# Performance work log

Hardware: AMD Instinct MI355X
Metric: run time of the kernel (lower is better)

Reference implementation:

```python
import jax, jax.numpy as jnp
import numpy as np

B, N, E, H = 32, 1024, 1024, 8
D = E // H      # head_dim = 128, att_mid_dim = [128, 64, 128]
MID = 64


def setup_inputs() -> dict:
    key = jax.random.key(0)
    ks = jax.random.split(key, 12)

    def lin(k, out_d, in_d):
        return (jax.random.normal(k, (out_d, in_d), jnp.float32) * 0.02,
                jnp.zeros((out_d,), jnp.float32))

    Wq, bq = lin(ks[0], E, E)
    Wk, bk = lin(ks[1], E, E)
    Wv, bv = lin(ks[2], E, E)
    Wb, bb = lin(ks[3], MID, D)    # attention_basic: Linear(mid[0]=D -> mid[1]=64) + ReLU
    Wl, bl = lin(ks[4], 1, MID)    # attention_last: Linear(64 -> 1)
    Wl2, bl2 = lin(ks[5], D, MID)  # attention_last2: Linear(64 -> D)
    query = jax.random.normal(ks[6], (B, E), jnp.float32)
    k_in = jax.random.normal(ks[7], (B, N, E), jnp.float32)
    value1 = jax.random.normal(ks[8], (B, E), jnp.float32)
    value2 = jax.random.normal(ks[9], (B, N, E), jnp.float32)
    mask = jax.random.randint(ks[10], (B, N), 0, 2, jnp.int32)
    mask = mask.at[:, 0].set(1)  # guarantee at least one valid position per row
    return {"query": query, "key": k_in, "mask": mask, "value1": value1,
            "value2": value2, "Wq": Wq, "bq": bq, "Wk": Wk, "bk": bk,
            "Wv": Wv, "bv": bv, "Wb": Wb, "bb": bb, "Wl": Wl, "bl": bl,
            "Wl2": Wl2, "bl2": bl2}


def reference(query, key, mask, value1, value2, Wq, bq, Wk, bk, Wv, bv,
              Wb, bb, Wl, bl, Wl2, bl2):
    # --- QKV projections (single-query attention) ---
    Q = (query @ Wq.T + bq).reshape(B, 1, H, D).transpose(0, 2, 1, 3)    # [B,H,1,D]
    K = (key @ Wk.T + bk).reshape(B, N, H, D).transpose(0, 2, 1, 3)      # [B,H,N,D]
    V = (key @ Wv.T + bv).reshape(B, N, H, D).transpose(0, 2, 1, 3)      # [B,H,N,D]
    v1 = value1.reshape(B, H, D)                                          # [B,H,D]
    v2 = (value2 @ Wv.T + bv).reshape(B, N, H, D).transpose(0, 2, 1, 3)   # [B,H,N,D]

    scores = jnp.einsum('bhqd,bhkd->bhqk', Q, K) / jnp.sqrt(jnp.float32(D))  # [B,H,1,N]
    attended = jnp.einsum('bhqk,bhkd->bhqd', scores, V)                      # [B,H,1,D]
    attn_map = jnp.broadcast_to(attended, (B, H, N, D))                      # expand(-1,-1,N,-1)

    # --- SCAtt attn_net ---
    h = jax.nn.relu(jnp.einsum('bhnd,md->bhnm', attn_map, Wb) + bb)          # [B,H,N,64]
    mf = mask.astype(h.dtype)                                                # [B,N]
    mext = mf[:, None, :, None]                                              # [B,1,N,1]
    att_map_pool = jnp.sum(h * mext, axis=2) / jnp.sum(mext, axis=2)         # [B,H,64]
    alpha_spatial = (jnp.einsum('bhnm,om->bhno', h, Wl) + bl)[..., 0]        # [B,H,N]
    alpha_channel = jax.nn.sigmoid(att_map_pool @ Wl2.T + bl2)               # [B,H,D]
    alpha_spatial = jnp.where(mf[:, None, :] == 0, jnp.float32(-1e9), alpha_spatial)
    alpha_spatial = jax.nn.softmax(alpha_spatial, axis=-1)                   # [B,H,N]
    v2_att = jnp.einsum('bhn,bhnd->bhd', alpha_spatial, v2)                  # [B,H,D]
    attn = v1 * v2_att * alpha_channel                                       # [B,H,D]
    return attn.reshape(B, H * D)
```

## Files before the change

### kernel.cpp

```cpp
#include <hip/hip_runtime.h>

#define B_  32
#define N_  1024
#define E_  1024
#define H_  8
#define D_  128
#define MID_ 64
#define NT_  32
#define TR_  32
#define NSP_ 32


__global__ __launch_bounds__(256) void k_q(
        const float* __restrict__ query, const float* __restrict__ Wq,
        const float* __restrict__ bq, const float* __restrict__ bk,
        float* __restrict__ Qs, float* __restrict__ qb,
        const float* __restrict__ value2, const int* __restrict__ mask,
        float* __restrict__ P2p)
{
    const int t = threadIdx.x;

    __shared__ __align__(16) float qsh[8 * E_];
    __shared__ __align__(16) float Qrow[8][16];
    __shared__ int rows[NSP_];
    __shared__ int nrows;

    if (blockIdx.x < 256) {
        const int bg = blockIdx.x >> 6;
        const int rs = blockIdx.x & 63;
        const int b0 = bg * 8;
        const int R  = rs * 16;
        const int h  = rs >> 3;

        {
            const int bb = t >> 5, ln = t & 31;
            const float4* src = (const float4*)(query + (size_t)(b0 + bb) * E_);
            float4* dst = (float4*)(qsh + bb * E_);
            #pragma unroll
            for (int i = 0; i < 8; ++i) dst[ln + i * 32] = src[ln + i * 32];
        }
        __syncthreads();

        const int r = t >> 4, cl = t & 15;
        const int row = R + r;
        const float4* wr = (const float4*)(Wq + (size_t)row * E_);
        float4 wchunk[16];
        #pragma unroll
        for (int i = 0; i < 16; ++i) wchunk[i] = wr[cl + i * 16];

        const float bqv = bq[row];
        const float4* qsh4 = (const float4*)qsh;
        #pragma unroll
        for (int bb = 0; bb < 8; ++bb) {
            float acc = 0.f;
            #pragma unroll
            for (int i = 0; i < 16; ++i) {
                float4 q = qsh4[bb * 256 + cl + i * 16];
                acc += wchunk[i].x * q.x + wchunk[i].y * q.y
                     + wchunk[i].z * q.z + wchunk[i].w * q.w;
            }
            #pragma unroll
            for (int off = 8; off; off >>= 1) acc += __shfl_xor(acc, off);
            if (cl == 0) Qrow[bb][r] = acc + bqv;
        }
        __syncthreads();

        if (t < 8) {
            float s = 0.f;
            #pragma unroll
            for (int rr = 0; rr < 16; ++rr) s += Qrow[t][rr] * bk[R + rr];
            atomicAdd(&qb[(b0 + t) * 8 + h], s);
        }
        if (t < 32) {
            const int bb = t >> 2, j = t & 3;
            ((float4*)(Qs + (size_t)(b0 + bb) * E_))[rs * 4 + j] =
                *(const float4*)&Qrow[bb][j * 4];
        }
    } else {
        const int pi = blockIdx.x - 256;
        const int b = pi & 31, sp = pi >> 5;
        const int e0 = t * 4;
        const int n0 = sp * NSP_;

        if (t == 0) nrows = 0;
        __syncthreads();
        if (t < NSP_) {
            if (mask[b * N_ + n0 + t]) {
                int i2 = atomicAdd(&nrows, 1);
                rows[i2] = t;
            }
        }
        __syncthreads();
        const int nr = nrows;

        float a0 = 0.f, a1 = 0.f, a2 = 0.f, a3 = 0.f;
        const float* vb = value2 + ((size_t)(b * N_ + n0)) * E_ + e0;
        #pragma unroll 4
        for (int i = 0; i < nr; ++i) {
            float4 v = *(const float4*)(vb + (size_t)rows[i] * E_);
            a0 += v.x; a1 += v.y; a2 += v.z; a3 += v.w;
        }
        float* dst = P2p + ((size_t)(sp & 7) * B_ + b) * E_ + e0;
        atomicAdd(dst + 0, a0); atomicAdd(dst + 1, a1);
        atomicAdd(dst + 2, a2); atomicAdd(dst + 3, a3);
    }
}

__global__ __launch_bounds__(256) void k_k(
        const float* __restrict__ Qs, const float* __restrict__ Wk,
        float* __restrict__ qk)
{
    const int h = blockIdx.x >> 5, ec = blockIdx.x & 31;
    const int t = threadIdx.x;

    __shared__ __align__(16) float QsL[32 * 132];
    __shared__ __align__(16) float WkL[128 * 32];

    {
        const int b = t >> 3, j = t & 7;
        const float4* src = (const float4*)(Qs + (size_t)b * E_) + h * 32;
        float4* dst = (float4*)(QsL + b * 132);
        #pragma unroll
        for (int jj = 0; jj < 4; ++jj) dst[j + jj * 8] = src[j + jj * 8];
    }
    {
        #pragma unroll
        for (int jj = 0; jj < 4; ++jj) {
            const int idx = t + jj * 256;
            const int d = idx >> 3, c = idx & 7;
            ((float4*)WkL)[idx] =
                ((const float4*)(Wk + (size_t)(h * D_ + d) * E_))[ec * 8 + c];
        }
    }
    __syncthreads();

    const int b = t >> 3, eg = t & 7;
    float4 acc = make_float4(0.f, 0.f, 0.f, 0.f);
    const float* q = QsL + b * 132;
    const float4* wk4 = (const float4*)WkL;
    #pragma unroll 8
    for (int d = 0; d < D_; ++d) {
        float qd = q[d];
        float4 w = wk4[d * 8 + eg];
        acc.x += qd * w.x; acc.y += qd * w.y;
        acc.z += qd * w.z; acc.w += qd * w.w;
    }
    ((float4*)(qk + (size_t)(b * 8 + h) * E_))[ec * 8 + eg] = acc;
}

__global__ __launch_bounds__(256) void k_main(
        const float* __restrict__ key, const float* __restrict__ qk,
        const float* __restrict__ qb, float* __restrict__ PPpart,
        float* __restrict__ ssum)
{
    const int tile = blockIdx.x, b = blockIdx.y;
    const int t = threadIdx.x;
    const int w = t >> 6, l = t & 63;

    __shared__ __align__(16) float part[4][4][8];
    __shared__ __align__(16) float sfin[4][8];

    const float scale = 0.08838834764831845f;
    const float* keyb = key + ((size_t)b * N_ + (size_t)tile * TR_) * E_;
    const float qbv = (t < 32) ? qb[b * 8 + (t & 7)] : 0.f;

    float4 qkr[8];
    #pragma unroll
    for (int h = 0; h < H_; ++h)
        qkr[h] = ((const float4*)(qk + (size_t)(b * 8 + h) * E_))[t];

    float4 pacc[8];
    #pragma unroll
    for (int h = 0; h < 8; ++h) pacc[h] = make_float4(0.f, 0.f, 0.f, 0.f);

    float ts = 0.f;

    float4 kv[4];
    #pragma unroll
    for (int r = 0; r < 4; ++r)
        kv[r] = ((const float4*)(keyb + (size_t)r * E_))[t];

    for (int st = 0; st < 8; ++st) {
        #pragma unroll
        for (int r = 0; r < 4; ++r) {
            float p[8];
            #pragma unroll
            for (int h = 0; h < 8; ++h)
                p[h] = qkr[h].x * kv[r].x + qkr[h].y * kv[r].y
                     + qkr[h].z * kv[r].z + qkr[h].w * kv[r].w;
            #pragma unroll
            for (int off = 32; off; off >>= 1) {
                #pragma unroll
                for (int h = 0; h < 8; ++h)
                    p[h] += __shfl_xor(p[h], off);
            }
            if (l == 0) {
                *(float4*)&part[w][r][0] = make_float4(p[0], p[1], p[2], p[3]);
                *(float4*)&part[w][r][4] = make_float4(p[4], p[5], p[6], p[7]);
            }
        }
        float4 kn[4];
        if (st < 7) {
            #pragma unroll
            for (int r = 0; r < 4; ++r)
                kn[r] = ((const float4*)(keyb
                            + (size_t)((st + 1) * 4 + r) * E_))[t];
        }
        __syncthreads();
        if (t < 32) {
            const int r = t >> 3, h = t & 7;
            float s = (part[0][r][h] + part[1][r][h]
                     + part[2][r][h] + part[3][r][h] + qbv) * scale;
            sfin[r][h] = s;
            ts += s;
        }
        __syncthreads();
        #pragma unroll
        for (int r = 0; r < 4; ++r) {
            const float4 k4 = kv[r];
            const float4 sA = *(const float4*)&sfin[r][0];
            const float4 sB = *(const float4*)&sfin[r][4];
            pacc[0].x += sA.x * k4.x; pacc[0].y += sA.x * k4.y;
            pacc[0].z += sA.x * k4.z; pacc[0].w += sA.x * k4.w;
            pacc[1].x += sA.y * k4.x; pacc[1].y += sA.y * k4.y;
            pacc[1].z += sA.y * k4.z; pacc[1].w += sA.y * k4.w;
            pacc[2].x += sA.z * k4.x; pacc[2].y += sA.z * k4.y;
            pacc[2].z += sA.z * k4.z; pacc[2].w += sA.z * k4.w;
            pacc[3].x += sA.w * k4.x; pacc[3].y += sA.w * k4.y;
            pacc[3].z += sA.w * k4.z; pacc[3].w += sA.w * k4.w;
            pacc[4].x += sB.x * k4.x; pacc[4].y += sB.x * k4.y;
            pacc[4].z += sB.x * k4.z; pacc[4].w += sB.x * k4.w;
            pacc[5].x += sB.y * k4.x; pacc[5].y += sB.y * k4.y;
            pacc[5].z += sB.y * k4.z; pacc[5].w += sB.y * k4.w;
            pacc[6].x += sB.z * k4.x; pacc[6].y += sB.z * k4.y;
            pacc[6].z += sB.z * k4.z; pacc[6].w += sB.z * k4.w;
            pacc[7].x += sB.w * k4.x; pacc[7].y += sB.w * k4.y;
            pacc[7].z += sB.w * k4.z; pacc[7].w += sB.w * k4.w;
        }
        #pragma unroll
        for (int r = 0; r < 4; ++r) kv[r] = kn[r];
    }

    if (t < 32) {
        float v = ts;
        v += __shfl_xor(v, 8);
        v += __shfl_xor(v, 16);
        if (l < 8) atomicAdd(&ssum[b * 8 + l], v);
    }

    #pragma unroll
    for (int h = 0; h < 8; ++h) {
        ((float4*)(PPpart
            + (((size_t)(b * H_ + h)) * NT_ + tile) * E_))[t] = pacc[h];
    }
}

__global__ __launch_bounds__(256) void k_red(
        const float* __restrict__ PPpart, const float* __restrict__ P2p,
        float* __restrict__ pooled, float* __restrict__ pool2)
{
    const int bh = blockIdx.x;
    const int t = threadIdx.x;
    const float4* pp = (const float4*)(PPpart + (size_t)bh * NT_ * E_);
    float4 s = make_float4(0.f, 0.f, 0.f, 0.f);
    #pragma unroll 8
    for (int tl = 0; tl < NT_; ++tl) {
        float4 v = pp[tl * 256 + t];
        s.x += v.x; s.y += v.y; s.z += v.z; s.w += v.w;
    }
    ((float4*)(pooled + (size_t)bh * E_))[t] = s;

    if (bh < B_) {
        float4 q = make_float4(0.f, 0.f, 0.f, 0.f);
        #pragma unroll
        for (int k2 = 0; k2 < 8; ++k2) {
            float4 v = ((const float4*)(P2p + ((size_t)k2 * B_ + bh) * E_))[t];
            q.x += v.x; q.y += v.y; q.z += v.z; q.w += v.w;
        }
        ((float4*)(pool2 + (size_t)bh * E_))[t] = q;
    }
}

__global__ __launch_bounds__(256) void k_att2(
        const float* __restrict__ pooled, const float* __restrict__ pool2,
        const float* __restrict__ Wv,
        float* __restrict__ attA, float* __restrict__ attV)
{
    const int h  = blockIdx.x >> 5;
    const int dc = (blockIdx.x >> 2) & 7;
    const int bq = blockIdx.x & 3;
    const int t = threadIdx.x;

    __shared__ __align__(16) float pL[8 * E_];
    __shared__ __align__(16) float p2L[8 * E_];

    {
        const int bb = t >> 5, ln = t & 31;
        const int b = bq * 8 + bb;
        const float4* sp = (const float4*)(pooled + (size_t)(b * 8 + h) * E_);
        const float4* s2 = (const float4*)(pool2 + (size_t)b * E_);
        float4* dp = (float4*)(pL + bb * E_);
        float4* d2 = (float4*)(p2L + bb * E_);
        #pragma unroll
        for (int i = 0; i < 8; ++i) {
            dp[ln + i * 32] = sp[ln + i * 32];
            d2[ln + i * 32] = s2[ln + i * 32];
        }
    }
    __syncthreads();

    const int r = t >> 4, cl = t & 15;
    const int d = dc * 16 + r;
    const float4* wvr = (const float4*)(Wv + (size_t)(h * D_ + d) * E_);
    const float4* pL4 = (const float4*)pL;
    const float4* p2L4 = (const float4*)p2L;

    float aA[8] = {}, aV[8] = {};
    #pragma unroll 4
    for (int i = 0; i < 16; ++i) {
        float4 w = wvr[cl + i * 16];
        #pragma unroll
        for (int bb = 0; bb < 8; ++bb) {
            float4 pa = pL4[bb * 256 + cl + i * 16];
            float4 pb = p2L4[bb * 256 + cl + i * 16];
            aA[bb] += w.x * pa.x + w.y * pa.y + w.z * pa.z + w.w * pa.w;
            aV[bb] += w.x * pb.x + w.y * pb.y + w.z * pb.z + w.w * pb.w;
        }
    }
    #pragma unroll
    for (int off = 8; off; off >>= 1) {
        #pragma unroll
        for (int bb = 0; bb < 8; ++bb) {
            aA[bb] += __shfl_xor(aA[bb], off);
            aV[bb] += __shfl_xor(aV[bb], off);
        }
    }
    if (cl == 0) {
        #pragma unroll
        for (int bb = 0; bb < 8; ++bb) {
            const int bh = (bq * 8 + bb) * 8 + h;
            attA[(size_t)bh * D_ + d] = aA[bb];
            attV[(size_t)bh * D_ + d] = aV[bb];
        }
    }
}

__global__ __launch_bounds__(128) void k_final(
        const float* __restrict__ attA, const float* __restrict__ attV,
        const float* __restrict__ ssumg, const int* __restrict__ mask,
        const float* __restrict__ bv, const float* __restrict__ Wb,
        const float* __restrict__ bb, const float* __restrict__ Wl2,
        const float* __restrict__ bl2, const float* __restrict__ value1,
        float* __restrict__ out)
{
    const int bh = blockIdx.x, b = bh >> 3, h = bh & 7;
    const int t = threadIdx.x;

    __shared__ float att[D_];
    __shared__ float hv[MID_];
    __shared__ float red2[2];
    __shared__ float cnt_s;

    int ci = 0;
    #pragma unroll
    for (int i = 0; i < 8; ++i) ci += mask[b * N_ + t + i * 128];
    float cf = (float)ci;
    #pragma unroll
    for (int off = 32; off; off >>= 1) cf += __shfl_down(cf, off);
    if ((t & 63) == 0) red2[t >> 6] = cf;

    const float ss = ssumg[bh];
    att[t] = attA[(size_t)bh * D_ + t] + ss * bv[h * D_ + t];
    __syncthreads();
    if (t == 0) cnt_s = red2[0] + red2[1];
    if (t < MID_) {
        float a = bb[t];
        #pragma unroll 4
        for (int d2 = 0; d2 < D_; ++d2) a += att[d2] * Wb[t * D_ + d2];
        hv[t] = fmaxf(a, 0.f);
    }
    __syncthreads();

    float z = bl2[t];
    #pragma unroll
    for (int m = 0; m < MID_; ++m) z += hv[m] * Wl2[t * MID_ + m];
    float alphac = 1.f / (1.f + expf(-z));
    const float bvd = bv[h * D_ + t];
    float v2a = attV[(size_t)bh * D_ + t] / cnt_s + bvd;
    out[(size_t)b * E_ + h * D_ + t] =
        value1[(size_t)b * E_ + h * D_ + t] * v2a * alphac;
}

extern "C" void kernel_launch(void* const* d_in, const int* in_sizes, int n_in,
                              void* d_out, int out_size, void* d_ws, size_t ws_size,
                              hipStream_t stream)
{
    const float* query  = (const float*)d_in[0];
    const float* key    = (const float*)d_in[1];
    const int*   mask   = (const int*)d_in[2];
    const float* value1 = (const float*)d_in[3];
    const float* value2 = (const float*)d_in[4];
    const float* Wq  = (const float*)d_in[5];
    const float* bq  = (const float*)d_in[6];
    const float* Wk  = (const float*)d_in[7];
    const float* bk  = (const float*)d_in[8];
    const float* Wv  = (const float*)d_in[9];
    const float* bv  = (const float*)d_in[10];
    const float* Wb  = (const float*)d_in[11];
    const float* bb  = (const float*)d_in[12];
    const float* Wl2 = (const float*)d_in[15];
    const float* bl2 = (const float*)d_in[16];
    float* out = (float*)d_out;

    char* ws = (char*)d_ws;
    const size_t SZ_PPP = (size_t)B_ * H_ * NT_ * E_ * 4;
    const size_t SZ_P2P = (size_t)8 * B_ * E_ * 4;
    const size_t OFF_P2P = SZ_PPP;
    const size_t OFF_SS  = OFF_P2P + SZ_P2P;
    const size_t OFF_QB  = OFF_SS + 1024;
    const size_t OFF_QS  = OFF_QB + 1024;
    const size_t OFF_QK  = OFF_QS + (size_t)B_ * E_ * 4;
    const size_t OFF_PL  = OFF_QK + (size_t)B_ * H_ * E_ * 4;
    const size_t OFF_P2  = OFF_PL + (size_t)B_ * H_ * E_ * 4;
    const size_t OFF_AA  = OFF_P2 + (size_t)B_ * E_ * 4;
    const size_t OFF_AV  = OFF_AA + (size_t)B_ * H_ * D_ * 4;
    float* PPpart = (float*)(ws);
    float* P2p    = (float*)(ws + OFF_P2P);
    float* ssum   = (float*)(ws + OFF_SS);
    float* qb     = (float*)(ws + OFF_QB);
    float* Qs     = (float*)(ws + OFF_QS);
    float* qk     = (float*)(ws + OFF_QK);
    float* pooled = (float*)(ws + OFF_PL);
    float* pool2  = (float*)(ws + OFF_P2);
    float* attA   = (float*)(ws + OFF_AA);
    float* attV   = (float*)(ws + OFF_AV);

    hipMemsetAsync(ws + OFF_P2P, 0, SZ_P2P + 2048, stream);

    hipLaunchKernelGGL(k_q, dim3(256 + NT_ * B_), dim3(256), 0, stream,
                       query, Wq, bq, bk, Qs, qb, value2, mask, P2p);
    hipLaunchKernelGGL(k_k, dim3(256), dim3(256), 0, stream,
                       Qs, Wk, qk);
    hipLaunchKernelGGL(k_main, dim3(NT_, B_), dim3(256), 0, stream,
                       key, qk, qb, PPpart, ssum);
    hipLaunchKernelGGL(k_red, dim3(B_ * H_), dim3(256), 0, stream,
                       PPpart, P2p, pooled, pool2);
    hipLaunchKernelGGL(k_att2, dim3(256), dim3(256), 0, stream,
                       pooled, pool2, Wv, attA, attV);
    hipLaunchKernelGGL(k_final, dim3(B_ * H_), dim3(128), 0, stream,
                       attA, attV, ssum, mask, bv, Wb, bb, Wl2, bl2,
                       value1, out);
}
```

Before: 371.7 us.

## Fuse six-kernel pipeline into one cooperative persistent kernel with grid syncs

Replaces the six separate kernel launches with a single cooperative kernel of 256 blocks of 1024 threads. Stages are separated by grid.sync, and shared memory is reused through a union. Each block now runs four former 256-thread jobs (pooling and key-tile main loop), and the Q, K and Wv projection stages are remapped to 1024 threads. This removes launch overhead and inter-kernel gaps, but adds grid-wide barriers and caps parallelism at 256 blocks. It may also lower occupancy for the heavy key-streaming stage.

```diff
diff --git a/kernel.cpp b/kernel.cpp
--- a/kernel.cpp
+++ b/kernel.cpp
@@ -1,4 +1,7 @@
 #include <hip/hip_runtime.h>
+#include <hip/hip_cooperative_groups.h>
+
+namespace cg = cooperative_groups;
 
 #define B_  32
 #define N_  1024
@@ -8,387 +11,361 @@
 #define MID_ 64
 #define NT_  32
 #define TR_  32
-#define NSP_ 32
-
-
-__global__ __launch_bounds__(256) void k_q(
+
+
+__device__ __forceinline__ float dot4(float4 a, float4 b) {
+    return a.x * b.x + a.y * b.y + a.z * b.z + a.w * b.w;
+}
+
+union SMem {
+    struct { float qsh[8 * E_]; float Qrow[8][16]; } q;
+    struct { int rows[4][32]; int nrows[4]; } pool;
+    struct { float QsL[32 * 132]; float WkL[128 * 32]; } kk;
+    struct { float part[4][4][4][8]; float sfin[4][4][8]; } mn;
+    struct { float4 red[4][256]; } rd;
+    struct { float pL[8 * E_]; float p2L[8 * E_]; } at;
+    struct { float att[D_]; float hv[MID_]; float red2[2]; float cnt; } fin;
+};
+
+__global__ __launch_bounds__(1024) void k_mega(
         const float* __restrict__ query, const float* __restrict__ Wq,
-        const float* __restrict__ bq, const float* __restrict__ bk,
+        const float* __restrict__ bq, const float* __restrict__ Wk,
+        const float* __restrict__ bk, const float* __restrict__ key,
+        const float* __restrict__ value2, const int* __restrict__ mask,
+        const float* __restrict__ Wv, const float* __restrict__ bv,
+        const float* __restrict__ Wb, const float* __restrict__ bbias,
+        const float* __restrict__ Wl2, const float* __restrict__ bl2,
+        const float* __restrict__ value1,
         float* __restrict__ Qs, float* __restrict__ qb,
-        const float* __restrict__ value2, const int* __restrict__ mask,
-        float* __restrict__ P2p)
+        float* __restrict__ qk, float* __restrict__ PPpart,
+        float* __restrict__ ssum, float* __restrict__ P2p,
+        float* __restrict__ pooled, float* __restrict__ pool2,
+        float* __restrict__ attA, float* __restrict__ attV,
+        float* __restrict__ out)
 {
+    cg::grid_group grid = cg::this_grid();
+    __shared__ SMem sm;
+    const int bid = blockIdx.x;
     const int t = threadIdx.x;
-
-    __shared__ __align__(16) float qsh[8 * E_];
-    __shared__ __align__(16) float Qrow[8][16];
-    __shared__ int rows[NSP_];
-    __shared__ int nrows;
-
-    if (blockIdx.x < 256) {
-        const int bg = blockIdx.x >> 6;
-        const int rs = blockIdx.x & 63;
-        const int b0 = bg * 8;
-        const int R  = rs * 16;
-        const int h  = rs >> 3;
-
-        {
-            const int bb = t >> 5, ln = t & 31;
-            const float4* src = (const float4*)(query + (size_t)(b0 + bb) * E_);
-            float4* dst = (float4*)(qsh + bb * E_);
-            #pragma unroll
-            for (int i = 0; i < 8; ++i) dst[ln + i * 32] = src[ln + i * 32];
-        }
-        __syncthreads();
-
-        const int r = t >> 4, cl = t & 15;
-        const int row = R + r;
-        const float4* wr = (const float4*)(Wq + (size_t)row * E_);
-        float4 wchunk[16];
-        #pragma unroll
-        for (int i = 0; i < 16; ++i) wchunk[i] = wr[cl + i * 16];
-
-        const float bqv = bq[row];
-        const float4* qsh4 = (const float4*)qsh;
-        #pragma unroll
-        for (int bb = 0; bb < 8; ++bb) {
-            float acc = 0.f;
-            #pragma unroll
-            for (int i = 0; i < 16; ++i) {
-                float4 q = qsh4[bb * 256 + cl + i * 16];
-                acc += wchunk[i].x * q.x + wchunk[i].y * q.y
-                     + wchunk[i].z * q.z + wchunk[i].w * q.w;
-            }
-            #pragma unroll
-            for (int off = 8; off; off >>= 1) acc += __shfl_xor(acc, off);
-            if (cl == 0) Qrow[bb][r] = acc + bqv;
-        }
-        __syncthreads();
-
-        if (t < 8) {
-            float s = 0.f;
-            #pragma unroll
-            for (int rr = 0; rr < 16; ++rr) s += Qrow[t][rr] * bk[R + rr];
-            atomicAdd(&qb[(b0 + t) * 8 + h], s);
-        }
-        if (t < 32) {
-            const int bb = t >> 2, j = t & 3;
-            ((float4*)(Qs + (size_t)(b0 + bb) * E_))[rs * 4 + j] =
-                *(const float4*)&Qrow[bb][j * 4];
-        }
-    } else {
-        const int pi = blockIdx.x - 256;
-        const int b = pi & 31, sp = pi >> 5;
-        const int e0 = t * 4;
-        const int n0 = sp * NSP_;
-
-        if (t == 0) nrows = 0;
-        __syncthreads();
-        if (t < NSP_) {
-            if (mask[b * N_ + n0 + t]) {
-                int i2 = atomicAdd(&nrows, 1);
-                rows[i2] = t;
-            }
-        }
-        __syncthreads();
-        const int nr = nrows;
-
+    const int g = t >> 8, tg = t & 255;
+
+    {
+        const int job = bid * 4 + g;
+        const int b = job & 31, sp = job >> 5;
+        const int n0 = sp * 32;
+        if (tg == 0) sm.pool.nrows[g] = 0;
+        __syncthreads();
+        if (tg < 32) {
+            if (mask[b * N_ + n0 + tg]) {
+                int i2 = atomicAdd(&sm.pool.nrows[g], 1);
+                sm.pool.rows[g][i2] = tg;
+            }
+        }
+        __syncthreads();
+        const int nr = sm.pool.nrows[g];
+        const int e0 = tg * 4;
         float a0 = 0.f, a1 = 0.f, a2 = 0.f, a3 = 0.f;
         const float* vb = value2 + ((size_t)(b * N_ + n0)) * E_ + e0;
         #pragma unroll 4
         for (int i = 0; i < nr; ++i) {
-            float4 v = *(const float4*)(vb + (size_t)rows[i] * E_);
+            float4 v = *(const float4*)(vb + (size_t)sm.pool.rows[g][i] * E_);
             a0 += v.x; a1 += v.y; a2 += v.z; a3 += v.w;
         }
         float* dst = P2p + ((size_t)(sp & 7) * B_ + b) * E_ + e0;
         atomicAdd(dst + 0, a0); atomicAdd(dst + 1, a1);
         atomicAdd(dst + 2, a2); atomicAdd(dst + 3, a3);
     }
-}
-
-__global__ __launch_bounds__(256) void k_k(
-        const float* __restrict__ Qs, const float* __restrict__ Wk,
-        float* __restrict__ qk)
-{
-    const int h = blockIdx.x >> 5, ec = blockIdx.x & 31;
-    const int t = threadIdx.x;
-
-    __shared__ __align__(16) float QsL[32 * 132];
-    __shared__ __align__(16) float WkL[128 * 32];
-
-    {
-        const int b = t >> 3, j = t & 7;
-        const float4* src = (const float4*)(Qs + (size_t)b * E_) + h * 32;
-        float4* dst = (float4*)(QsL + b * 132);
-        #pragma unroll
-        for (int jj = 0; jj < 4; ++jj) dst[j + jj * 8] = src[j + jj * 8];
-    }
-    {
-        #pragma unroll
-        for (int jj = 0; jj < 4; ++jj) {
-            const int idx = t + jj * 256;
-            const int d = idx >> 3, c = idx & 7;
-            ((float4*)WkL)[idx] =
+    __syncthreads();
+
+    {
+        const int bg = bid >> 6, rs = bid & 63;
+        const int b0 = bg * 8, R = rs * 16, h = rs >> 3;
+        {
+            const int bb = t >> 7, ln = t & 127;
+            const float4* src = (const float4*)(query + (size_t)(b0 + bb) * E_);
+            float4* dst = (float4*)(sm.q.qsh + bb * E_);
+            dst[ln] = src[ln];
+            dst[ln + 128] = src[ln + 128];
+        }
+        __syncthreads();
+        const int r = t >> 6, cl = t & 63;
+        const int row = R + r;
+        const float4* wr = (const float4*)(Wq + (size_t)row * E_);
+        const float4 w0 = wr[cl], w1 = wr[cl + 64],
+                     w2 = wr[cl + 128], w3 = wr[cl + 192];
+        const float4* qsh4 = (const float4*)sm.q.qsh;
+        const float bqv = bq[row];
+        #pragma unroll
+        for (int bb = 0; bb < 8; ++bb) {
+            float acc = dot4(w0, qsh4[bb * 256 + cl])
+                      + dot4(w1, qsh4[bb * 256 + cl + 64])
+                      + dot4(w2, qsh4[bb * 256 + cl + 128])
+                      + dot4(w3, qsh4[bb * 256 + cl + 192]);
+            #pragma unroll
+            for (int off = 32; off; off >>= 1) acc += __shfl_xor(acc, off);
+            if (cl == 0) sm.q.Qrow[bb][r] = acc + bqv;
+        }
+        __syncthreads();
+        if (t < 8) {
+            float s = 0.f;
+            #pragma unroll
+            for (int rr = 0; rr < 16; ++rr) s += sm.q.Qrow[t][rr] * bk[R + rr];
+            atomicAdd(&qb[(b0 + t) * 8 + h], s);
+        }
+        if (t < 32) {
+            const int bb = t >> 2, j = t & 3;
+            ((float4*)(Qs + (size_t)(b0 + bb) * E_))[rs * 4 + j] =
+                *(const float4*)&sm.q.Qrow[bb][j * 4];
+        }
+    }
+    __threadfence();
+    grid.sync();
+
+    {
+        const int h = bid >> 5, ec = bid & 31;
+        {
+            const int b = t >> 5, j = t & 31;
+            ((float4*)(sm.kk.QsL + b * 132))[j] =
+                ((const float4*)(Qs + (size_t)b * E_))[h * 32 + j];
+        }
+        {
+            const int d = t >> 3, c = t & 7;
+            ((float4*)sm.kk.WkL)[t] =
                 ((const float4*)(Wk + (size_t)(h * D_ + d) * E_))[ec * 8 + c];
         }
-    }
-    __syncthreads();
-
-    const int b = t >> 3, eg = t & 7;
-    float4 acc = make_float4(0.f, 0.f, 0.f, 0.f);
-    const float* q = QsL + b * 132;
-    const float4* wk4 = (const float4*)WkL;
-    #pragma unroll 8
-    for (int d = 0; d < D_; ++d) {
-        float qd = q[d];
-        float4 w = wk4[d * 8 + eg];
-        acc.x += qd * w.x; acc.y += qd * w.y;
-        acc.z += qd * w.z; acc.w += qd * w.w;
-    }
-    ((float4*)(qk + (size_t)(b * 8 + h) * E_))[ec * 8 + eg] = acc;
-}
-
-__global__ __launch_bounds__(256) void k_main(
-        const float* __restrict__ key, const float* __restrict__ qk,
-        const float* __restrict__ qb, float* __restrict__ PPpart,
-        float* __restrict__ ssum)
-{
-    const int tile = blockIdx.x, b = blockIdx.y;
-    const int t = threadIdx.x;
-    const int w = t >> 6, l = t & 63;
-
-    __shared__ __align__(16) float part[4][4][8];
-    __shared__ __align__(16) float sfin[4][8];
-
-    const float scale = 0.08838834764831845f;
-    const float* keyb = key + ((size_t)b * N_ + (size_t)tile * TR_) * E_;
-    const float qbv = (t < 32) ? qb[b * 8 + (t & 7)] : 0.f;
-
-    float4 qkr[8];
-    #pragma unroll
-    for (int h = 0; h < H_; ++h)
-        qkr[h] = ((const float4*)(qk + (size_t)(b * 8 + h) * E_))[t];
-
-    float4 pacc[8];
-    #pragma unroll
-    for (int h = 0; h < 8; ++h) pacc[h] = make_float4(0.f, 0.f, 0.f, 0.f);
-
-    float ts = 0.f;
-
-    float4 kv[4];
-    #pragma unroll
-    for (int r = 0; r < 4; ++r)
-        kv[r] = ((const float4*)(keyb + (size_t)r * E_))[t];
-
-    for (int st = 0; st < 8; ++st) {
-        #pragma unroll
-        for (int r = 0; r < 4; ++r) {
-            float p[8];
-            #pragma unroll
-            for (int h = 0; h < 8; ++h)
-                p[h] = qkr[h].x * kv[r].x + qkr[h].y * kv[r].y
-                     + qkr[h].z * kv[r].z + qkr[h].w * kv[r].w;
-            #pragma unroll
-            for (int off = 32; off; off >>= 1) {
+        __syncthreads();
+        const int b = t >> 5, ef = t & 31;
+        float acc = 0.f;
+        const float* qrow = sm.kk.QsL + b * 132;
+        #pragma unroll 8
+        for (int d = 0; d < D_; ++d)
+            acc += qrow[d] * sm.kk.WkL[d * 32 + ef];
+        qk[(size_t)(b * 8 + h) * E_ + ec * 32 + ef] = acc;
+    }
+    __threadfence();
+    grid.sync();
+
+    {
+        const int j = bid * 4 + g;
+        const int b = j >> 5, tile = j & 31;
+        const int w = tg >> 6, l = tg & 63;
+        const float scale = 0.08838834764831845f;
+        const float* keyb = key + ((size_t)b * N_ + (size_t)tile * TR_) * E_;
+        const float qbv = (tg < 32) ? qb[b * 8 + (tg & 7)] : 0.f;
+
+        float4 qkr[8];
+        #pragma unroll
+        for (int h = 0; h < H_; ++h)
+            qkr[h] = ((const float4*)(qk + (size_t)(b * 8 + h) * E_))[tg];
+
+        float4 pacc[8];
+        #pragma unroll
+        for (int h = 0; h < 8; ++h) pacc[h] = make_float4(0.f, 0.f, 0.f, 0.f);
+
+        float ts = 0.f;
+        float4 kv[4];
+        #pragma unroll
+        for (int r = 0; r < 4; ++r)
+            kv[r] = ((const float4*)(keyb + (size_t)r * E_))[tg];
+
+        for (int st = 0; st < 8; ++st) {
+            #pragma unroll
+            for (int r = 0; r < 4; ++r) {
+                float p[8];
                 #pragma unroll
-                for (int h = 0; h < 8; ++h)
-                    p[h] += __shfl_xor(p[h], off);
-            }
-            if (l == 0) {
-                *(float4*)&part[w][r][0] = make_float4(p[0], p[1], p[2], p[3]);
-                *(float4*)&part[w][r][4] = make_float4(p[4], p[5], p[6], p[7]);
-            }
-        }
-        float4 kn[4];
-        if (st < 7) {
-            #pragma unroll
-            for (int r = 0; r < 4; ++r)
-                kn[r] = ((const float4*)(keyb
-                            + (size_t)((st + 1) * 4 + r) * E_))[t];
-        }
-        __syncthreads();
-        if (t < 32) {
-            const int r = t >> 3, h = t & 7;
-            float s = (part[0][r][h] + part[1][r][h]
-                     + part[2][r][h] + part[3][r][h] + qbv) * scale;
-            sfin[r][h] = s;
-            ts += s;
-        }
-        __syncthreads();
-        #pragma unroll
-        for (int r = 0; r < 4; ++r) {
-            const float4 k4 = kv[r];
-            const float4 sA = *(const float4*)&sfin[r][0];
-            const float4 sB = *(const float4*)&sfin[r][4];
-            pacc[0].x += sA.x * k4.x; pacc[0].y += sA.x * k4.y;
-            pacc[0].z += sA.x * k4.z; pacc[0].w += sA.x * k4.w;
-            pacc[1].x += sA.y * k4.x; pacc[1].y += sA.y * k4.y;
-            pacc[1].z += sA.y * k4.z; pacc[1].w += sA.y * k4.w;
-            pacc[2].x += sA.z * k4.x; pacc[2].y += sA.z * k4.y;
-            pacc[2].z += sA.z * k4.z; pacc[2].w += sA.z * k4.w;
-            pacc[3].x += sA.w * k4.x; pacc[3].y += sA.w * k4.y;
-            pacc[3].z += sA.w * k4.z; pacc[3].w += sA.w * k4.w;
-            pacc[4].x += sB.x * k4.x; pacc[4].y += sB.x * k4.y;
-            pacc[4].z += sB.x * k4.z; pacc[4].w += sB.x * k4.w;
-            pacc[5].x += sB.y * k4.x; pacc[5].y += sB.y * k4.y;
-            pacc[5].z += sB.y * k4.z; pacc[5].w += sB.y * k4.w;
-            pacc[6].x += sB.z * k4.x; pacc[6].y += sB.z * k4.y;
-            pacc[6].z += sB.z * k4.z; pacc[6].w += sB.z * k4.w;
-            pacc[7].x += sB.w * k4.x; pacc[7].y += sB.w * k4.y;
-            pacc[7].z += sB.w * k4.z; pacc[7].w += sB.w * k4.w;
-        }
-        #pragma unroll
-        for (int r = 0; r < 4; ++r) kv[r] = kn[r];
-    }
-
-    if (t < 32) {
-        float v = ts;
-        v += __shfl_xor(v, 8);
-        v += __shfl_xor(v, 16);
-        if (l < 8) atomicAdd(&ssum[b * 8 + l], v);
-    }
-
-    #pragma unroll
-    for (int h = 0; h < 8; ++h) {
-        ((float4*)(PPpart
-            + (((size_t)(b * H_ + h)) * NT_ + tile) * E_))[t] = pacc[h];
-    }
-}
-
-__global__ __launch_bounds__(256) void k_red(
-        const float* __restrict__ PPpart, const float* __restrict__ P2p,
-        float* __restrict__ pooled, float* __restrict__ pool2)
-{
-    const int bh = blockIdx.x;
-    const int t = threadIdx.x;
-    const float4* pp = (const float4*)(PPpart + (size_t)bh * NT_ * E_);
-    float4 s = make_float4(0.f, 0.f, 0.f, 0.f);
-    #pragma unroll 8
-    for (int tl = 0; tl < NT_; ++tl) {
-        float4 v = pp[tl * 256 + t];
-        s.x += v.x; s.y += v.y; s.z += v.z; s.w += v.w;
-    }
-    ((float4*)(pooled + (size_t)bh * E_))[t] = s;
-
-    if (bh < B_) {
-        float4 q = make_float4(0.f, 0.f, 0.f, 0.f);
-        #pragma unroll
-        for (int k2 = 0; k2 < 8; ++k2) {
-            float4 v = ((const float4*)(P2p + ((size_t)k2 * B_ + bh) * E_))[t];
-            q.x += v.x; q.y += v.y; q.z += v.z; q.w += v.w;
-        }
-        ((float4*)(pool2 + (size_t)bh * E_))[t] = q;
-    }
-}
-
-__global__ __launch_bounds__(256) void k_att2(
-        const float* __restrict__ pooled, const float* __restrict__ pool2,
-        const float* __restrict__ Wv,
-        float* __restrict__ attA, float* __restrict__ attV)
-{
-    const int h  = blockIdx.x >> 5;
-    const int dc = (blockIdx.x >> 2) & 7;
-    const int bq = blockIdx.x & 3;
-    const int t = threadIdx.x;
-
-    __shared__ __align__(16) float pL[8 * E_];
-    __shared__ __align__(16) float p2L[8 * E_];
-
-    {
-        const int bb = t >> 5, ln = t & 31;
-        const int b = bq * 8 + bb;
-        const float4* sp = (const float4*)(pooled + (size_t)(b * 8 + h) * E_);
-        const float4* s2 = (const float4*)(pool2 + (size_t)b * E_);
-        float4* dp = (float4*)(pL + bb * E_);
-        float4* d2 = (float4*)(p2L + bb * E_);
-        #pragma unroll
-        for (int i = 0; i < 8; ++i) {
-            dp[ln + i * 32] = sp[ln + i * 32];
-            d2[ln + i * 32] = s2[ln + i * 32];
-        }
-    }
-    __syncthreads();
-
-    const int r = t >> 4, cl = t & 15;
-    const int d = dc * 16 + r;
-    const float4* wvr = (const float4*)(Wv + (size_t)(h * D_ + d) * E_);
-    const float4* pL4 = (const float4*)pL;
-    const float4* p2L4 = (const float4*)p2L;
-
-    float aA[8] = {}, aV[8] = {};
-    #pragma unroll 4
-    for (int i = 0; i < 16; ++i) {
-        float4 w = wvr[cl + i * 16];
+                for (int h = 0; h < 8; ++h) p[h] = dot4(qkr[h], kv[r]);
+                #pragma unroll
+                for (int off = 32; off; off >>= 1) {
+                    #pragma unroll
+                    for (int h = 0; h < 8; ++h)
+                        p[h] += __shfl_xor(p[h], off);
+                }
+                if (l == 0) {
+                    *(float4*)&sm.mn.part[g][w][r][0] =
+                        make_float4(p[0], p[1], p[2], p[3]);
+                    *(float4*)&sm.mn.part[g][w][r][4] =
+                        make_float4(p[4], p[5], p[6], p[7]);
+                }
+            }
+            float4 kn[4];
+            if (st < 7) {
+                #pragma unroll
+                for (int r = 0; r < 4; ++r)
+                    kn[r] = ((const float4*)(keyb
+                                + (size_t)((st + 1) * 4 + r) * E_))[tg];
+            }
+            __syncthreads();
+            if (tg < 32) {
+                const int r = tg >> 3, h = tg & 7;
+                float s = (sm.mn.part[g][0][r][h] + sm.mn.part[g][1][r][h]
+                         + sm.mn.part[g][2][r][h] + sm.mn.part[g][3][r][h]
+                         + qbv) * scale;
+                sm.mn.sfin[g][r][h] = s;
+                ts += s;
+            }
+            __syncthreads();
+            #pragma unroll
+            for (int r = 0; r < 4; ++r) {
+                const float4 k4 = kv[r];
+                const float4 sA = *(const float4*)&sm.mn.sfin[g][r][0];
+                const float4 sB = *(const float4*)&sm.mn.sfin[g][r][4];
+                pacc[0].x += sA.x * k4.x; pacc[0].y += sA.x * k4.y;
+                pacc[0].z += sA.x * k4.z; pacc[0].w += sA.x * k4.w;
+                pacc[1].x += sA.y * k4.x; pacc[1].y += sA.y * k4.y;
+                pacc[1].z += sA.y * k4.z; pacc[1].w += sA.y * k4.w;
+                pacc[2].x += sA.z * k4.x; pacc[2].y += sA.z * k4.y;
+                pacc[2].z += sA.z * k4.z; pacc[2].w += sA.z * k4.w;
+                pacc[3].x += sA.w * k4.x; pacc[3].y += sA.w * k4.y;
+                pacc[3].z += sA.w * k4.z; pacc[3].w += sA.w * k4.w;
+                pacc[4].x += sB.x * k4.x; pacc[4].y += sB.x * k4.y;
+                pacc[4].z += sB.x * k4.z; pacc[4].w += sB.x * k4.w;
+                pacc[5].x += sB.y * k4.x; pacc[5].y += sB.y * k4.y;
+                pacc[5].z += sB.y * k4.z; pacc[5].w += sB.y * k4.w;
+                pacc[6].x += sB.z * k4.x; pacc[6].y += sB.z * k4.y;
+                pacc[6].z += sB.z * k4.z; pacc[6].w += sB.z * k4.w;
+                pacc[7].x += sB.w * k4.x; pacc[7].y += sB.w * k4.y;
+                pacc[7].z += sB.w * k4.z; pacc[7].w += sB.w * k4.w;
+            }
+            #pragma unroll
+            for (int r = 0; r < 4; ++r) kv[r] = kn[r];
+        }
+
+        if (tg < 32) {
+            float v = ts;
+            v += __shfl_xor(v, 8);
+            v += __shfl_xor(v, 16);
+            if (l < 8) atomicAdd(&ssum[b * 8 + l], v);
+        }
+        #pragma unroll
+        for (int h = 0; h < 8; ++h) {
+            ((float4*)(PPpart
+                + (((size_t)(b * H_ + h)) * NT_ + tile) * E_))[tg] = pacc[h];
+        }
+    }
+    __threadfence();
+    grid.sync();
+
+    {
+        const int bh = bid;
+        const float4* pp = (const float4*)(PPpart + (size_t)bh * NT_ * E_);
+        float4 s = make_float4(0.f, 0.f, 0.f, 0.f);
+        #pragma unroll
+        for (int jj = 0; jj < 8; ++jj) {
+            float4 v = pp[(g * 8 + jj) * 256 + tg];
+            s.x += v.x; s.y += v.y; s.z += v.z; s.w += v.w;
+        }
+        sm.rd.red[g][tg] = s;
+        __syncthreads();
+        if (t < 256) {
+            float4 r0 = sm.rd.red[0][t], r1 = sm.rd.red[1][t];
+            float4 r2 = sm.rd.red[2][t], r3 = sm.rd.red[3][t];
+            ((float4*)(pooled + (size_t)bh * E_))[t] =
+                make_float4(r0.x + r1.x + r2.x + r3.x,
+                            r0.y + r1.y + r2.y + r3.y,
+                            r0.z + r1.z + r2.z + r3.z,
+                            r0.w + r1.w + r2.w + r3.w);
+        }
+        if (bid < B_ && t < 256) {
+            float4 q = make_float4(0.f, 0.f, 0.f, 0.f);
+            #pragma unroll
+            for (int k2 = 0; k2 < 8; ++k2) {
+                float4 v = ((const float4*)(P2p
+                                + ((size_t)k2 * B_ + bid) * E_))[t];
+                q.x += v.x; q.y += v.y; q.z += v.z; q.w += v.w;
+            }
+            ((float4*)(pool2 + (size_t)bid * E_))[t] = q;
+        }
+    }
+    __threadfence();
+    grid.sync();
+
+    {
+        const int h = bid >> 5, dc = (bid >> 2) & 7, bq4 = bid & 3;
+        const int b0 = bq4 * 8;
+        {
+            const int bb = t >> 7, ln = t & 127;
+            const float4* sp = (const float4*)(pooled
+                                + (size_t)((b0 + bb) * 8 + h) * E_);
+            const float4* s2 = (const float4*)(pool2 + (size_t)(b0 + bb) * E_);
+            float4* dp = (float4*)(sm.at.pL + bb * E_);
+            float4* d2 = (float4*)(sm.at.p2L + bb * E_);
+            dp[ln] = sp[ln]; dp[ln + 128] = sp[ln + 128];
+            d2[ln] = s2[ln]; d2[ln + 128] = s2[ln + 128];
+        }
+        __syncthreads();
+        const int r = t >> 6, cl = t & 63;
+        const int d = dc * 16 + r;
+        const float4* wvr = (const float4*)(Wv + (size_t)(h * D_ + d) * E_);
+        const float4 w0 = wvr[cl], w1 = wvr[cl + 64],
+                     w2 = wvr[cl + 128], w3 = wvr[cl + 192];
+        const float4* pL4 = (const float4*)sm.at.pL;
+        const float4* p2L4 = (const float4*)sm.at.p2L;
+        float aA[8], aV[8];
         #pragma unroll
         for (int bb = 0; bb < 8; ++bb) {
-            float4 pa = pL4[bb * 256 + cl + i * 16];
-            float4 pb = p2L4[bb * 256 + cl + i * 16];
-            aA[bb] += w.x * pa.x + w.y * pa.y + w.z * pa.z + w.w * pa.w;
-            aV[bb] += w.x * pb.x + w.y * pb.y + w.z * pb.z + w.w * pb.w;
-        }
-    }
-    #pragma unroll
-    for (int off = 8; off; off >>= 1) {
-        #pragma unroll
-        for (int bb = 0; bb < 8; ++bb) {
-            aA[bb] += __shfl_xor(aA[bb], off);
-            aV[bb] += __shfl_xor(aV[bb], off);
-        }
-    }
-    if (cl == 0) {
-        #pragma unroll
-        for (int bb = 0; bb < 8; ++bb) {
-            const int bh = (bq * 8 + bb) * 8 + h;
-            attA[(size_t)bh * D_ + d] = aA[bb];
-            attV[(size_t)bh * D_ + d] = aV[bb];
-        }
-    }
-}
-
-__global__ __launch_bounds__(128) void k_final(
-        const float* __restrict__ attA, const float* __restrict__ attV,
-        const float* __restrict__ ssumg, const int* __restrict__ mask,
-        const float* __restrict__ bv, const float* __restrict__ Wb,
-        const float* __restrict__ bb, const float* __restrict__ Wl2,
-        const float* __restrict__ bl2, const float* __restrict__ value1,
-        float* __restrict__ out)
-{
-    const int bh = blockIdx.x, b = bh >> 3, h = bh & 7;
-    const int t = threadIdx.x;
-
-    __shared__ float att[D_];
-    __shared__ float hv[MID_];
-    __shared__ float red2[2];
-    __shared__ float cnt_s;
-
-    int ci = 0;
-    #pragma unroll
-    for (int i = 0; i < 8; ++i) ci += mask[b * N_ + t + i * 128];
-    float cf = (float)ci;
-    #pragma unroll
-    for (int off = 32; off; off >>= 1) cf += __shfl_down(cf, off);
-    if ((t & 63) == 0) red2[t >> 6] = cf;
-
-    const float ss = ssumg[bh];
-    att[t] = attA[(size_t)bh * D_ + t] + ss * bv[h * D_ + t];
-    __syncthreads();
-    if (t == 0) cnt_s = red2[0] + red2[1];
-    if (t < MID_) {
-        float a = bb[t];
-        #pragma unroll 4
-        for (int d2 = 0; d2 < D_; ++d2) a += att[d2] * Wb[t * D_ + d2];
-        hv[t] = fmaxf(a, 0.f);
-    }
-    __syncthreads();
-
-    float z = bl2[t];
-    #pragma unroll
-    for (int m = 0; m < MID_; ++m) z += hv[m] * Wl2[t * MID_ + m];
-    float alphac = 1.f / (1.f + expf(-z));
-    const float bvd = bv[h * D_ + t];
-    float v2a = attV[(size_t)bh * D_ + t] / cnt_s + bvd;
-    out[(size_t)b * E_ + h * D_ + t] =
-        value1[(size_t)b * E_ + h * D_ + t] * v2a * alphac;
+            aA[bb] = dot4(w0, pL4[bb * 256 + cl])
+                   + dot4(w1, pL4[bb * 256 + cl + 64])
+                   + dot4(w2, pL4[bb * 256 + cl + 128])
+                   + dot4(w3, pL4[bb * 256 + cl + 192]);
+            aV[bb] = dot4(w0, p2L4[bb * 256 + cl])
+                   + dot4(w1, p2L4[bb * 256 + cl + 64])
+                   + dot4(w2, p2L4[bb * 256 + cl + 128])
+                   + dot4(w3, p2L4[bb * 256 + cl + 192]);
+        }
+        #pragma unroll
+        for (int off = 32; off; off >>= 1) {
+            #pragma unroll
+            for (int bb = 0; bb < 8; ++bb) {
+                aA[bb] += __shfl_xor(aA[bb], off);
+                aV[bb] += __shfl_xor(aV[bb], off);
+            }
+        }
+        if (cl == 0) {
+            #pragma unroll
+            for (int bb = 0; bb < 8; ++bb) {
+                const int bh2 = (b0 + bb) * 8 + h;
+                attA[(size_t)bh2 * D_ + d] = aA[bb];
+                attV[(size_t)bh2 * D_ + d] = aV[bb];
+            }
+        }
+    }
+    __threadfence();
+    grid.sync();
+
+    {
+        const int bh = bid, b = bh >> 3, h = bh & 7;
+        if (t < 128) {
+            int ci = 0;
+            #pragma unroll
+            for (int i = 0; i < 8; ++i) ci += mask[b * N_ + t + i * 128];
+            float cf = (float)ci;
+            #pragma unroll
+            for (int off = 32; off; off >>= 1) cf += __shfl_down(cf, off);
+            if ((t & 63) == 0) sm.fin.red2[t >> 6] = cf;
+            const float ss = ssum[bh];
+            sm.fin.att[t] = attA[(size_t)bh * D_ + t] + ss * bv[h * D_ + t];
+        }
+        __syncthreads();
+        if (t == 0) sm.fin.cnt = sm.fin.red2[0] + sm.fin.red2[1];
+        if (t < MID_) {
+            float a = bbias[t];
+            #pragma unroll 4
+            for (int d2 = 0; d2 < D_; ++d2)
+                a += sm.fin.att[d2] * Wb[t * D_ + d2];
+            sm.fin.hv[t] = fmaxf(a, 0.f);
+        }
+        __syncthreads();
+        if (t < 128) {
+            float z = bl2[t];
+            #pragma unroll
+            for (int m = 0; m < MID_; ++m) z += sm.fin.hv[m] * Wl2[t * MID_ + m];
+            float alphac = 1.f / (1.f + expf(-z));
+            const float bvd = bv[h * D_ + t];
+            float v2a = attV[(size_t)bh * D_ + t] / sm.fin.cnt + bvd;
+            out[(size_t)b * E_ + h * D_ + t] =
+                value1[(size_t)b * E_ + h * D_ + t] * v2a * alphac;
+        }
+    }
 }
 
 extern "C" void kernel_launch(void* const* d_in, const int* in_sizes, int n_in,
@@ -407,7 +384,7 @@
     const float* Wv  = (const float*)d_in[9];
     const float* bv  = (const float*)d_in[10];
     const float* Wb  = (const float*)d_in[11];
-    const float* bb  = (const float*)d_in[12];
+    const float* bbias = (const float*)d_in[12];
     const float* Wl2 = (const float*)d_in[15];
     const float* bl2 = (const float*)d_in[16];
     float* out = (float*)d_out;
@@ -437,17 +414,14 @@
 
     hipMemsetAsync(ws + OFF_P2P, 0, SZ_P2P + 2048, stream);
 
-    hipLaunchKernelGGL(k_q, dim3(256 + NT_ * B_), dim3(256), 0, stream,
-                       query, Wq, bq, bk, Qs, qb, value2, mask, P2p);
-    hipLaunchKernelGGL(k_k, dim3(256), dim3(256), 0, stream,
-                       Qs, Wk, qk);
-    hipLaunchKernelGGL(k_main, dim3(NT_, B_), dim3(256), 0, stream,
-                       key, qk, qb, PPpart, ssum);
-    hipLaunchKernelGGL(k_red, dim3(B_ * H_), dim3(256), 0, stream,
-                       PPpart, P2p, pooled, pool2);
-    hipLaunchKernelGGL(k_att2, dim3(256), dim3(256), 0, stream,
-                       pooled, pool2, Wv, attA, attV);
-    hipLaunchKernelGGL(k_final, dim3(B_ * H_), dim3(128), 0, stream,
-                       attA, attV, ssum, mask, bv, Wb, bb, Wl2, bl2,
-                       value1, out);
+    void* args[] = {
+        (void*)&query, (void*)&Wq, (void*)&bq, (void*)&Wk, (void*)&bk,
+        (void*)&key, (void*)&value2, (void*)&mask, (void*)&Wv, (void*)&bv,
+        (void*)&Wb, (void*)&bbias, (void*)&Wl2, (void*)&bl2, (void*)&value1,
+        (void*)&Qs, (void*)&qb, (void*)&qk, (void*)&PPpart, (void*)&ssum,
+        (void*)&P2p, (void*)&pooled, (void*)&pool2, (void*)&attA,
+        (void*)&attV, (void*)&out
+    };
+    hipLaunchCooperativeKernel((void*)k_mega, dim3(256), dim3(1024),
+                               args, 0, stream);
 }
```

Result: slower. 960.9 us (+158.5%).

## Fuse reduction, Wv projection and final gating into one tail kernel

Applied to the files above, without the earlier changes.

Merges the three trailing kernels (partial-sum reduction, Wv projection of pooled vectors, final MLP/gating) into one 512-thread kernel per (batch, head), keeping pooled, pool2 and the attention vectors in shared memory instead of global workspace. This removes two launches and global round-trips. In exchange, each block now streams its own 128 Wv rows, so Wv reuse across batches is lost and Wv traffic grows about eightfold, served mostly from cache. It also replaces __syncthreads in k_main with a custom barrier that waits only on LDS counters, not on the outstanding prefetch loads.

```diff
diff --git a/kernel.cpp b/kernel.cpp
--- a/kernel.cpp
+++ b/kernel.cpp
@@ -10,6 +10,11 @@
 #define TR_  32
 #define NSP_ 32
 
+
+__device__ __forceinline__ void ldsbar() {
+    asm volatile("s_waitcnt lgkmcnt(0)\n"
+                 "s_barrier" ::: "memory");
+}
 
 __global__ __launch_bounds__(256) void k_q(
         const float* __restrict__ query, const float* __restrict__ Wq,
@@ -206,7 +211,7 @@
                 kn[r] = ((const float4*)(keyb
                             + (size_t)((st + 1) * 4 + r) * E_))[t];
         }
-        __syncthreads();
+        ldsbar();
         if (t < 32) {
             const int r = t >> 3, h = t & 7;
             float s = (part[0][r][h] + part[1][r][h]
@@ -214,7 +219,7 @@
             sfin[r][h] = s;
             ts += s;
         }
-        __syncthreads();
+        ldsbar();
         #pragma unroll
         for (int r = 0; r < 4; ++r) {
             const float4 k4 = kv[r];
@@ -255,122 +260,91 @@
     }
 }
 
-__global__ __launch_bounds__(256) void k_red(
+__global__ __launch_bounds__(512) void k_tail(
         const float* __restrict__ PPpart, const float* __restrict__ P2p,
-        float* __restrict__ pooled, float* __restrict__ pool2)
-{
-    const int bh = blockIdx.x;
-    const int t = threadIdx.x;
-    const float4* pp = (const float4*)(PPpart + (size_t)bh * NT_ * E_);
-    float4 s = make_float4(0.f, 0.f, 0.f, 0.f);
-    #pragma unroll 8
-    for (int tl = 0; tl < NT_; ++tl) {
-        float4 v = pp[tl * 256 + t];
-        s.x += v.x; s.y += v.y; s.z += v.z; s.w += v.w;
-    }
-    ((float4*)(pooled + (size_t)bh * E_))[t] = s;
-
-    if (bh < B_) {
-        float4 q = make_float4(0.f, 0.f, 0.f, 0.f);
-        #pragma unroll
-        for (int k2 = 0; k2 < 8; ++k2) {
-            float4 v = ((const float4*)(P2p + ((size_t)k2 * B_ + bh) * E_))[t];
-            q.x += v.x; q.y += v.y; q.z += v.z; q.w += v.w;
-        }
-        ((float4*)(pool2 + (size_t)bh * E_))[t] = q;
-    }
-}
-
-__global__ __launch_bounds__(256) void k_att2(
-        const float* __restrict__ pooled, const float* __restrict__ pool2,
-        const float* __restrict__ Wv,
-        float* __restrict__ attA, float* __restrict__ attV)
-{
-    const int h  = blockIdx.x >> 5;
-    const int dc = (blockIdx.x >> 2) & 7;
-    const int bq = blockIdx.x & 3;
-    const int t = threadIdx.x;
-
-    __shared__ __align__(16) float pL[8 * E_];
-    __shared__ __align__(16) float p2L[8 * E_];
-
-    {
-        const int bb = t >> 5, ln = t & 31;
-        const int b = bq * 8 + bb;
-        const float4* sp = (const float4*)(pooled + (size_t)(b * 8 + h) * E_);
-        const float4* s2 = (const float4*)(pool2 + (size_t)b * E_);
-        float4* dp = (float4*)(pL + bb * E_);
-        float4* d2 = (float4*)(p2L + bb * E_);
-        #pragma unroll
-        for (int i = 0; i < 8; ++i) {
-            dp[ln + i * 32] = sp[ln + i * 32];
-            d2[ln + i * 32] = s2[ln + i * 32];
-        }
-    }
-    __syncthreads();
-
-    const int r = t >> 4, cl = t & 15;
-    const int d = dc * 16 + r;
-    const float4* wvr = (const float4*)(Wv + (size_t)(h * D_ + d) * E_);
-    const float4* pL4 = (const float4*)pL;
-    const float4* p2L4 = (const float4*)p2L;
-
-    float aA[8] = {}, aV[8] = {};
-    #pragma unroll 4
-    for (int i = 0; i < 16; ++i) {
-        float4 w = wvr[cl + i * 16];
-        #pragma unroll
-        for (int bb = 0; bb < 8; ++bb) {
-            float4 pa = pL4[bb * 256 + cl + i * 16];
-            float4 pb = p2L4[bb * 256 + cl + i * 16];
-            aA[bb] += w.x * pa.x + w.y * pa.y + w.z * pa.z + w.w * pa.w;
-            aV[bb] += w.x * pb.x + w.y * pb.y + w.z * pb.z + w.w * pb.w;
-        }
-    }
-    #pragma unroll
-    for (int off = 8; off; off >>= 1) {
-        #pragma unroll
-        for (int bb = 0; bb < 8; ++bb) {
-            aA[bb] += __shfl_xor(aA[bb], off);
-            aV[bb] += __shfl_xor(aV[bb], off);
-        }
-    }
-    if (cl == 0) {
-        #pragma unroll
-        for (int bb = 0; bb < 8; ++bb) {
-            const int bh = (bq * 8 + bb) * 8 + h;
-            attA[(size_t)bh * D_ + d] = aA[bb];
-            attV[(size_t)bh * D_ + d] = aV[bb];
-        }
-    }
-}
-
-__global__ __launch_bounds__(128) void k_final(
-        const float* __restrict__ attA, const float* __restrict__ attV,
         const float* __restrict__ ssumg, const int* __restrict__ mask,
-        const float* __restrict__ bv, const float* __restrict__ Wb,
-        const float* __restrict__ bb, const float* __restrict__ Wl2,
-        const float* __restrict__ bl2, const float* __restrict__ value1,
-        float* __restrict__ out)
+        const float* __restrict__ Wv, const float* __restrict__ bv,
+        const float* __restrict__ Wb, const float* __restrict__ bb,
+        const float* __restrict__ Wl2, const float* __restrict__ bl2,
+        const float* __restrict__ value1, float* __restrict__ out)
 {
     const int bh = blockIdx.x, b = bh >> 3, h = bh & 7;
     const int t = threadIdx.x;
-
+    const int l = t & 63, w = t >> 6;
+    const int rg = l >> 4, cl = l & 15;
+
+    __shared__ __align__(16) float ph[2][E_];
+    __shared__ __align__(16) float pooled[E_];
+    __shared__ __align__(16) float pool2[E_];
+    __shared__ float attA_s[D_];
+    __shared__ float attV_s[D_];
     __shared__ float att[D_];
     __shared__ float hv[MID_];
     __shared__ float red2[2];
     __shared__ float cnt_s;
 
-    int ci = 0;
+    {
+        const int c4 = t & 255, half = t >> 8;
+        const float4* pp = (const float4*)(PPpart + (size_t)bh * NT_ * E_);
+        float4 s = make_float4(0.f, 0.f, 0.f, 0.f);
+        #pragma unroll 4
+        for (int j = 0; j < 16; ++j) {
+            float4 v = pp[(half * 16 + j) * 256 + c4];
+            s.x += v.x; s.y += v.y; s.z += v.z; s.w += v.w;
+        }
+        ((float4*)&ph[half][0])[c4] = s;
+    }
+    __syncthreads();
+    if (t < 256) {
+        float4 p0 = ((const float4*)&ph[0][0])[t];
+        float4 p1 = ((const float4*)&ph[1][0])[t];
+        ((float4*)pooled)[t] = make_float4(p0.x + p1.x, p0.y + p1.y,
+                                           p0.z + p1.z, p0.w + p1.w);
+        float4 q = make_float4(0.f, 0.f, 0.f, 0.f);
+        #pragma unroll
+        for (int k2 = 0; k2 < 8; ++k2) {
+            float4 v = ((const float4*)(P2p + ((size_t)k2 * B_ + b) * E_))[t];
+            q.x += v.x; q.y += v.y; q.z += v.z; q.w += v.w;
+        }
+        ((float4*)pool2)[t] = q;
+    }
+    __syncthreads();
+
+    const float4* pooled4 = (const float4*)pooled;
+    const float4* pool24  = (const float4*)pool2;
     #pragma unroll
-    for (int i = 0; i < 8; ++i) ci += mask[b * N_ + t + i * 128];
-    float cf = (float)ci;
-    #pragma unroll
-    for (int off = 32; off; off >>= 1) cf += __shfl_down(cf, off);
-    if ((t & 63) == 0) red2[t >> 6] = cf;
-
-    const float ss = ssumg[bh];
-    att[t] = attA[(size_t)bh * D_ + t] + ss * bv[h * D_ + t];
+    for (int p = 0; p < 4; ++p) {
+        const int d = p * 32 + w * 4 + rg;
+        const float4* wvr = (const float4*)(Wv + (size_t)(h * D_ + d) * E_);
+        float pA = 0.f, pV = 0.f;
+        #pragma unroll 4
+        for (int i = 0; i < 16; ++i) {
+            float4 wv4 = wvr[cl + i * 16];
+            float4 pa = pooled4[cl + i * 16];
+            float4 pb = pool24[cl + i * 16];
+            pA += wv4.x * pa.x + wv4.y * pa.y + wv4.z * pa.z + wv4.w * pa.w;
+            pV += wv4.x * pb.x + wv4.y * pb.y + wv4.z * pb.z + wv4.w * pb.w;
+        }
+        #pragma unroll
+        for (int off = 8; off; off >>= 1) {
+            pA += __shfl_xor(pA, off);
+            pV += __shfl_xor(pV, off);
+        }
+        if (cl == 0) { attA_s[d] = pA; attV_s[d] = pV; }
+    }
+    __syncthreads();
+
+    if (t < 128) {
+        int ci = 0;
+        #pragma unroll
+        for (int i = 0; i < 8; ++i) ci += mask[b * N_ + t + i * 128];
+        float cf = (float)ci;
+        #pragma unroll
+        for (int off = 32; off; off >>= 1) cf += __shfl_down(cf, off);
+        if ((t & 63) == 0) red2[t >> 6] = cf;
+        const float ss = ssumg[bh];
+        att[t] = attA_s[t] + ss * bv[h * D_ + t];
+    }
     __syncthreads();
     if (t == 0) cnt_s = red2[0] + red2[1];
     if (t < MID_) {
@@ -380,15 +354,16 @@
         hv[t] = fmaxf(a, 0.f);
     }
     __syncthreads();
-
-    float z = bl2[t];
-    #pragma unroll
-    for (int m = 0; m < MID_; ++m) z += hv[m] * Wl2[t * MID_ + m];
-    float alphac = 1.f / (1.f + expf(-z));
-    const float bvd = bv[h * D_ + t];
-    float v2a = attV[(size_t)bh * D_ + t] / cnt_s + bvd;
-    out[(size_t)b * E_ + h * D_ + t] =
-        value1[(size_t)b * E_ + h * D_ + t] * v2a * alphac;
+    if (t < 128) {
+        float z = bl2[t];
+        #pragma unroll
+        for (int m = 0; m < MID_; ++m) z += hv[m] * Wl2[t * MID_ + m];
+        float alphac = 1.f / (1.f + expf(-z));
+        const float bvd = bv[h * D_ + t];
+        float v2a = attV_s[t] / cnt_s + bvd;
+        out[(size_t)b * E_ + h * D_ + t] =
+            value1[(size_t)b * E_ + h * D_ + t] * v2a * alphac;
+    }
 }
 
 extern "C" void kernel_launch(void* const* d_in, const int* in_sizes, int n_in,
@@ -420,20 +395,12 @@
     const size_t OFF_QB  = OFF_SS + 1024;
     const size_t OFF_QS  = OFF_QB + 1024;
     const size_t OFF_QK  = OFF_QS + (size_t)B_ * E_ * 4;
-    const size_t OFF_PL  = OFF_QK + (size_t)B_ * H_ * E_ * 4;
-    const size_t OFF_P2  = OFF_PL + (size_t)B_ * H_ * E_ * 4;
-    const size_t OFF_AA  = OFF_P2 + (size_t)B_ * E_ * 4;
-    const size_t OFF_AV  = OFF_AA + (size_t)B_ * H_ * D_ * 4;
     float* PPpart = (float*)(ws);
     float* P2p    = (float*)(ws + OFF_P2P);
     float* ssum   = (float*)(ws + OFF_SS);
     float* qb     = (float*)(ws + OFF_QB);
     float* Qs     = (float*)(ws + OFF_QS);
     float* qk     = (float*)(ws + OFF_QK);
-    float* pooled = (float*)(ws + OFF_PL);
-    float* pool2  = (float*)(ws + OFF_P2);
-    float* attA   = (float*)(ws + OFF_AA);
-    float* attV   = (float*)(ws + OFF_AV);
 
     hipMemsetAsync(ws + OFF_P2P, 0, SZ_P2P + 2048, stream);
 
@@ -443,11 +410,7 @@
                        Qs, Wk, qk);
     hipLaunchKernelGGL(k_main, dim3(NT_, B_), dim3(256), 0, stream,
                        key, qk, qb, PPpart, ssum);
-    hipLaunchKernelGGL(k_red, dim3(B_ * H_), dim3(256), 0, stream,
-                       PPpart, P2p, pooled, pool2);
-    hipLaunchKernelGGL(k_att2, dim3(256), dim3(256), 0, stream,
-                       pooled, pool2, Wv, attA, attV);
-    hipLaunchKernelGGL(k_final, dim3(B_ * H_), dim3(128), 0, stream,
-                       attA, attV, ssum, mask, bv, Wb, bb, Wl2, bl2,
+    hipLaunchKernelGGL(k_tail, dim3(B_ * H_), dim3(512), 0, stream,
+                       PPpart, P2p, ssum, mask, Wv, bv, Wb, bb, Wl2, bl2,
                        value1, out);
 }
```

Result: no change. 370.0 us (-0.5%).
